# Optimization experiments

Hardware: AMD Instinct MI355X
Metric: run time of the kernel (lower is better)

The kernel has to match this reference:

```python
import jax, jax.numpy as jnp
import numpy as np
from jax import lax

B, Ht, Wt, C, NH, KV, FF = 32, 32, 32, 768, 12, 16, 4
HD = C // NH
EPS = 1e-5


def setup_inputs() -> dict:
    key = jax.random.key(0)
    ks = jax.random.split(key, 12)
    rn = lambda k, s, sc=0.02: jax.random.normal(k, s, jnp.float32) * sc
    inp = {"x": jax.random.normal(ks[0], (B, Ht * Wt, C), jnp.float32)}
    inp["ln1_g"] = jnp.ones((C,), jnp.float32)
    inp["ln1_b"] = jnp.zeros((C,), jnp.float32)
    for i, nm in enumerate(["q", "k", "v"]):
        inp[f"dw_w_{nm}"] = rn(ks[1 + i], (C, 1, 3, 3), 0.1)
        inp[f"dw_b_{nm}"] = jnp.zeros((C,), jnp.float32)
        inp[f"bn_g_{nm}"] = jnp.ones((C,), jnp.float32)
        inp[f"bn_b_{nm}"] = jnp.zeros((C,), jnp.float32)
        inp[f"bn_m_{nm}"] = jnp.zeros((C,), jnp.float32)
        inp[f"bn_v_{nm}"] = jnp.ones((C,), jnp.float32)
        inp[f"W_{nm}"] = rn(ks[4 + i], (C, C))
        inp[f"b_{nm}"] = jnp.zeros((C,), jnp.float32)
    inp["ln2_g"] = jnp.ones((C,), jnp.float32)
    inp["ln2_b"] = jnp.zeros((C,), jnp.float32)
    inp["W1"] = rn(ks[7], (FF * C, C))
    inp["b1"] = jnp.zeros((FF * C,), jnp.float32)
    inp["W2"] = rn(ks[8], (C, FF * C))
    inp["b2"] = jnp.zeros((C,), jnp.float32)
    return inp


def _ln(x, g, b):
    m = jnp.mean(x, -1, keepdims=True)
    v = jnp.var(x, -1, keepdims=True)
    return (x - m) * lax.rsqrt(v + EPS) * g + b


def _dw_branch(x4, w, bias, g, bb, m, v, stride):
    # depthwise conv (groups=C) -> ELU -> BatchNorm (eval) -> b (h w) c
    y = lax.conv_general_dilated(
        x4, w, (stride, stride), [(1, 1), (1, 1)],
        feature_group_count=C,
        dimension_numbers=("NCHW", "OIHW", "NCHW"),
    ) + bias[None, :, None, None]
    y = jax.nn.elu(y)
    y = (y - m[None, :, None, None]) * lax.rsqrt(v + EPS)[None, :, None, None] \
        * g[None, :, None, None] + bb[None, :, None, None]
    return y.reshape(B, C, -1).transpose(0, 2, 1)  # (B, n, C)


def _heads(t, Wm, bm):
    t = t @ Wm.T + bm                         # (B, n, C)
    n = t.shape[1]
    return t.reshape(B, n, NH, HD).transpose(0, 2, 1, 3)  # (B, H, n, d)


def reference(x, ln1_g, ln1_b,
              dw_w_q, dw_b_q, bn_g_q, bn_b_q, bn_m_q, bn_v_q, W_q, b_q,
              dw_w_k, dw_b_k, bn_g_k, bn_b_k, bn_m_k, bn_v_k, W_k, b_k,
              dw_w_v, dw_b_v, bn_g_v, bn_b_v, bn_m_v, bn_v_v, W_v, b_v,
              ln2_g, ln2_b, W1, b1, W2, b2):
    xn = _ln(x, ln1_g, ln1_b)
    x4 = xn.transpose(0, 2, 1).reshape(B, C, Ht, Wt)
    q = _heads(_dw_branch(x4, dw_w_q, dw_b_q, bn_g_q, bn_b_q, bn_m_q, bn_v_q, 1), W_q, b_q)
    k = _heads(_dw_branch(x4, dw_w_k, dw_b_k, bn_g_k, bn_b_k, bn_m_k, bn_v_k, 2), W_k, b_k)
    v = _heads(_dw_branch(x4, dw_w_v, dw_b_v, bn_g_v, bn_b_v, bn_m_v, bn_v_v, 2), W_v, b_v)
    scale = 1.0 / (HD ** 0.5)
    attn = jnp.einsum("bhnd,bhmd->bhnm", q, k) * scale
    attn = jax.nn.softmax(attn, axis=-1)
    o = jnp.einsum("bhnm,bhmd->bhnd", attn, v)
    o = o.transpose(0, 2, 1, 3).reshape(B, Ht * Wt, C)
    x = x + o  # DropPath is identity at inference
    h = _ln(x, ln2_g, ln2_b)
    h = jax.nn.gelu(h @ W1.T + b1, approximate=False) @ W2.T + b2
    return x + h
```

## Files before the change

### kernel.cpp

```cpp
#include <hip/hip_runtime.h>
#include <math.h>

#define NB   32
#define C_   768
#define NQ   1024
#define NKV  256
#define NH_  12
#define HD_  64
#define FFC  3072
#define EPS_ 1e-5f

typedef __attribute__((ext_vector_type(8))) _Float16 f16x8;
typedef __attribute__((ext_vector_type(4))) _Float16 f16x4;
typedef __attribute__((ext_vector_type(2))) _Float16 f16x2;
typedef __attribute__((ext_vector_type(4))) float    f32x4;

__device__ __forceinline__ void gload_lds16(const void* g, void* l) {
  __builtin_amdgcn_global_load_lds((const __attribute__((address_space(1))) void*)g,
                                   (__attribute__((address_space(3))) void*)l, 16, 0, 0);
}

__device__ __forceinline__ float gelu_f(float x) {
  return x / (1.f + __expf(-1.5957691216f * (x + 0.044715f * x * x * x)));
}

__global__ __launch_bounds__(256)
void ln_fwd_kernel(const float* __restrict__ x, const float* __restrict__ g,
                   const float* __restrict__ b, _Float16* __restrict__ out) {
  const int row = blockIdx.x;
  const float* xr = x + (size_t)row * C_;
  const int t = threadIdx.x;
  float v0 = xr[t], v1 = xr[t + 256], v2 = xr[t + 512];
  float s = v0 + v1 + v2;
  float q = v0 * v0 + v1 * v1 + v2 * v2;
#pragma unroll
  for (int m = 1; m < 64; m <<= 1) { s += __shfl_xor(s, m); q += __shfl_xor(q, m); }
  __shared__ float ls[4], lq[4];
  const int w = t >> 6, lane = t & 63;
  if (lane == 0) { ls[w] = s; lq[w] = q; }
  __syncthreads();
  s = ls[0] + ls[1] + ls[2] + ls[3];
  q = lq[0] + lq[1] + lq[2] + lq[3];
  const float mean = s * (1.f / C_);
  const float rstd = rsqrtf(q * (1.f / C_) - mean * mean + EPS_);
  _Float16* orow = out + (size_t)row * C_;
  orow[t]       = (_Float16)((v0 - mean) * rstd * g[t]       + b[t]);
  orow[t + 256] = (_Float16)((v1 - mean) * rstd * g[t + 256] + b[t + 256]);
  orow[t + 512] = (_Float16)((v2 - mean) * rstd * g[t + 512] + b[t + 512]);
}

__global__ __launch_bounds__(256)
void resln2_kernel(const float* __restrict__ x, const _Float16* __restrict__ o,
                   const float* __restrict__ g, const float* __restrict__ bb,
                   float* __restrict__ xr_out, _Float16* __restrict__ h) {
  const int row = blockIdx.x;
  const float* xp = x + (size_t)row * C_;
  const _Float16* op = o + (size_t)row * C_;
  const int t = threadIdx.x;
  float v[3]; float s = 0.f, q = 0.f;
#pragma unroll
  for (int i = 0; i < 3; i++) {
    int c = t + i * 256;
    v[i] = xp[c] + (float)op[c];
    s += v[i]; q += v[i] * v[i];
  }
#pragma unroll
  for (int m = 1; m < 64; m <<= 1) { s += __shfl_xor(s, m); q += __shfl_xor(q, m); }
  __shared__ float ls[4], lq[4];
  const int w = t >> 6, lane = t & 63;
  if (lane == 0) { ls[w] = s; lq[w] = q; }
  __syncthreads();
  s = ls[0] + ls[1] + ls[2] + ls[3];
  q = lq[0] + lq[1] + lq[2] + lq[3];
  const float mean = s * (1.f / C_);
  const float rstd = rsqrtf(q * (1.f / C_) - mean * mean + EPS_);
#pragma unroll
  for (int i = 0; i < 3; i++) {
    int c = t + i * 256;
    xr_out[(size_t)row * C_ + c] = v[i];
    h[(size_t)row * C_ + c] = (_Float16)((v[i] - mean) * rstd * g[c] + bb[c]);
  }
}

#define SZ_CC (C_ * C_)
#define SZ_CF (FFC * C_)
__global__ void cast_all_kernel(const float* __restrict__ Wq, const float* __restrict__ Wk,
                                const float* __restrict__ Wv, const float* __restrict__ W1,
                                const float* __restrict__ W2,
                                _Float16* __restrict__ oq, _Float16* __restrict__ ok,
                                _Float16* __restrict__ ov, _Float16* __restrict__ o1,
                                _Float16* __restrict__ o2) {
  const int total = 3 * SZ_CC + 2 * SZ_CF;
  int i = blockIdx.x * 256 + threadIdx.x;
  int stride = gridDim.x * 256;
  for (; i < total; i += stride) {
    if (i < SZ_CC)                     oq[i] = (_Float16)Wq[i];
    else if (i < 2 * SZ_CC)            ok[i - SZ_CC] = (_Float16)Wk[i - SZ_CC];
    else if (i < 3 * SZ_CC)            ov[i - 2 * SZ_CC] = (_Float16)Wv[i - 2 * SZ_CC];
    else if (i < 3 * SZ_CC + SZ_CF)    o1[i - 3 * SZ_CC] = (_Float16)W1[i - 3 * SZ_CC];
    else                               o2[i - 3 * SZ_CC - SZ_CF] = (_Float16)W2[i - 3 * SZ_CC - SZ_CF];
  }
}

__global__ __launch_bounds__(256)
void vtrans_kernel(const _Float16* __restrict__ vbuf, _Float16* __restrict__ vT) {
  const int b = blockIdx.z;
  const int c = blockIdx.y * 256 + threadIdx.x;
  const int kvb = blockIdx.x * 64;
#pragma unroll
  for (int kk = 0; kk < 8; kk++) {
    int kv0 = kvb + kk * 8;
    f16x8 v;
#pragma unroll
    for (int j = 0; j < 8; j++)
      v[j] = vbuf[(size_t)((b << 8) + kv0 + j) * C_ + c];
    *(f16x8*)(vT + ((size_t)(b * C_ + c) << 8) + kv0) = v;
  }
}

struct DwP { const float *w, *bias, *g, *b, *m, *v; };

__device__ __forceinline__ float elu_f(float x) {
  return x > 0.f ? x : __expf(x) - 1.f;
}

__global__ __launch_bounds__(384)
void dw_fused_kernel(const _Float16* __restrict__ xn, DwP pq, DwP pk, DwP pv,
                     _Float16* __restrict__ oq, _Float16* __restrict__ ok,
                     _Float16* __restrict__ ov) {
  const int i = blockIdx.x;
  const int b = blockIdx.z;
  const int c0 = 2 * threadIdx.x;
  const _Float16* xb = xn + (size_t)b * NQ * C_ + c0;

  float wqx[9], wqy[9], wkx[9], wky[9], wvx[9], wvy[9];
#pragma unroll
  for (int u = 0; u < 9; u++) {
    wqx[u] = pq.w[c0 * 9 + u]; wqy[u] = pq.w[(c0 + 1) * 9 + u];
    wkx[u] = pk.w[c0 * 9 + u]; wky[u] = pk.w[(c0 + 1) * 9 + u];
    wvx[u] = pv.w[c0 * 9 + u]; wvy[u] = pv.w[(c0 + 1) * 9 + u];
  }
  const float skqx = rsqrtf(pq.v[c0] + EPS_) * pq.g[c0], bnqx = pq.b[c0] - pq.m[c0] * skqx;
  const float skqy = rsqrtf(pq.v[c0+1] + EPS_) * pq.g[c0+1], bnqy = pq.b[c0+1] - pq.m[c0+1] * skqy;
  const float skkx = rsqrtf(pk.v[c0] + EPS_) * pk.g[c0], bnkx = pk.b[c0] - pk.m[c0] * skkx;
  const float skky = rsqrtf(pk.v[c0+1] + EPS_) * pk.g[c0+1], bnky = pk.b[c0+1] - pk.m[c0+1] * skky;
  const float skvx = rsqrtf(pv.v[c0] + EPS_) * pv.g[c0], bnvx = pv.b[c0] - pv.m[c0] * skvx;
  const float skvy = rsqrtf(pv.v[c0+1] + EPS_) * pv.g[c0+1], bnvy = pv.b[c0+1] - pv.m[c0+1] * skvy;
  const float cbqx = pq.bias[c0], cbqy = pq.bias[c0+1];
  const float cbkx = pk.bias[c0], cbky = pk.bias[c0+1];
  const float cbvx = pv.bias[c0], cbvy = pv.bias[c0+1];

  float tx[5][5], ty[5][5];
  auto ldc = [&](int s, int iw) {
    const bool cv = (iw >= 0 && iw < 32);
#pragma unroll
    for (int u = 0; u < 5; u++) {
      int ih = 2 * i - 1 + u;
      if (cv && ih >= 0 && ih < 32) {
        f16x2 p = *(const f16x2*)&xb[(size_t)(ih * 32 + iw) * C_];
        tx[u][s] = (float)p[0]; ty[u][s] = (float)p[1];
      } else { tx[u][s] = 0.f; ty[u][s] = 0.f; }
    }
  };

#pragma unroll
  for (int j = 0; j < 16; j++) {
    if (j == 0) {
      ldc(0, -1); ldc(1, 0); ldc(2, 1); ldc(3, 2); ldc(4, 3);
    } else {
#pragma unroll
      for (int u = 0; u < 5; u++) {
        tx[u][0] = tx[u][2]; tx[u][1] = tx[u][3]; tx[u][2] = tx[u][4];
        ty[u][0] = ty[u][2]; ty[u][1] = ty[u][3]; ty[u][2] = ty[u][4];
      }
      ldc(3, 2 * j + 2); ldc(4, 2 * j + 3);
    }
    float akx = cbkx, aky = cbky, avx = cbvx, avy = cbvy;
#pragma unroll
    for (int u = 0; u < 3; u++)
#pragma unroll
      for (int vv = 0; vv < 3; vv++) {
        akx += tx[u][vv] * wkx[u * 3 + vv]; aky += ty[u][vv] * wky[u * 3 + vv];
        avx += tx[u][vv] * wvx[u * 3 + vv]; avy += ty[u][vv] * wvy[u * 3 + vv];
      }
    f16x2 kv2, vv2;
    kv2[0] = (_Float16)(elu_f(akx) * skkx + bnkx);
    kv2[1] = (_Float16)(elu_f(aky) * skky + bnky);
    vv2[0] = (_Float16)(elu_f(avx) * skvx + bnvx);
    vv2[1] = (_Float16)(elu_f(avy) * skvy + bnvy);
    *(f16x2*)&ok[((size_t)b * NKV + i * 16 + j) * C_ + c0] = kv2;
    *(f16x2*)&ov[((size_t)b * NKV + i * 16 + j) * C_ + c0] = vv2;
#pragma unroll
    for (int a = 0; a < 2; a++)
#pragma unroll
      for (int b2 = 0; b2 < 2; b2++) {
        float aqx = cbqx, aqy = cbqy;
#pragma unroll
        for (int u = 0; u < 3; u++)
#pragma unroll
          for (int vv = 0; vv < 3; vv++) {
            aqx += tx[a + u][b2 + vv] * wqx[u * 3 + vv];
            aqy += ty[a + u][b2 + vv] * wqy[u * 3 + vv];
          }
        f16x2 q2;
        q2[0] = (_Float16)(elu_f(aqx) * skqx + bnqx);
        q2[1] = (_Float16)(elu_f(aqy) * skqy + bnqy);
        *(f16x2*)&oq[((size_t)b * NQ + (2 * i + a) * 32 + (2 * j + b2)) * C_ + c0] = q2;
      }
  }
}

__device__ __forceinline__ void stage_tile(const _Float16* __restrict__ src, int ldk,
                                           int row0, int kt, _Float16* lds, int w, int lane) {
#pragma unroll
  for (int it = 0; it < 4; it++) {
    int cid = (it * 4 + w) * 64 + lane;
    int row = cid >> 3, kg = cid & 7;
    int kgs = kg ^ (row & 7);
    const _Float16* g = src + (size_t)(row0 + row) * ldk + kt * 64 + kgs * 8;
    gload_lds16((const void*)g, (void*)((char*)lds + (it * 4 + w) * 1024));
  }
}

template <int EPI>
__device__ __forceinline__
void gemm_core(const _Float16* __restrict__ A, const _Float16* __restrict__ Bw,
               const float* __restrict__ bias,
               _Float16* __restrict__ outh, float* __restrict__ outf,
               int N, int K, int m0, int n0) {
  __shared__ __align__(16) _Float16 As[128 * 64];
  __shared__ __align__(16) _Float16 Bs[128 * 64];
  const int tid = threadIdx.x, w = tid >> 6, lane = tid & 63;
  const int wm = w >> 1, wn = w & 1;

  f32x4 acc[4][4];
#pragma unroll
  for (int i = 0; i < 4; i++)
#pragma unroll
    for (int j = 0; j < 4; j++)
#pragma unroll
      for (int r = 0; r < 4; r++) acc[i][j][r] = 0.f;

  const int NKT = K >> 6;
  for (int kt = 0; kt < NKT; kt++) {
    stage_tile(A, K, m0, kt, As, w, lane);
    stage_tile(Bw, K, n0, kt, Bs, w, lane);
    __syncthreads();
    f16x8 af[4][2], bfr[4][2];
#pragma unroll
    for (int mi = 0; mi < 4; mi++)
#pragma unroll
      for (int kh = 0; kh < 2; kh++) {
        int row = wm * 64 + mi * 16 + (lane & 15);
        int kg = kh * 4 + (lane >> 4);
        af[mi][kh] = *(const f16x8*)&As[row * 64 + ((kg ^ (row & 7)) << 3)];
      }
#pragma unroll
    for (int ni = 0; ni < 4; ni++)
#pragma unroll
      for (int kh = 0; kh < 2; kh++) {
        int row = wn * 64 + ni * 16 + (lane & 15);
        int kg = kh * 4 + (lane >> 4);
        bfr[ni][kh] = *(const f16x8*)&Bs[row * 64 + ((kg ^ (row & 7)) << 3)];
      }
    __builtin_amdgcn_s_setprio(1);
#pragma unroll
    for (int mi = 0; mi < 4; mi++)
#pragma unroll
      for (int ni = 0; ni < 4; ni++)
#pragma unroll
        for (int kh = 0; kh < 2; kh++)
          acc[mi][ni] = __builtin_amdgcn_mfma_f32_16x16x32_f16(af[mi][kh], bfr[ni][kh],
                                                               acc[mi][ni], 0, 0, 0);
    __builtin_amdgcn_s_setprio(0);
    __syncthreads();
  }
#pragma unroll
  for (int mi = 0; mi < 4; mi++)
#pragma unroll
    for (int ni = 0; ni < 4; ni++) {
      int col = n0 + wn * 64 + ni * 16 + (lane & 15);
      float bv = bias[col];
#pragma unroll
      for (int r = 0; r < 4; r++) {
        int rowg = m0 + wm * 64 + mi * 16 + (lane >> 4) * 4 + r;
        float val = acc[mi][ni][r] + bv;
        size_t idx = (size_t)rowg * N + col;
        if (EPI == 0)      outh[idx] = (_Float16)val;
        else if (EPI == 1) outh[idx] = (_Float16)gelu_f(val);
        else               outf[idx] += val;
      }
    }
}

template <int EPI>
__global__ __launch_bounds__(256, 3)
void gemm_f16(const _Float16* __restrict__ A, const _Float16* __restrict__ Bw,
              const float* __restrict__ bias,
              _Float16* __restrict__ outh, float* __restrict__ outf,
              int M, int N, int K, int NT) {
  const int nwg = gridDim.x, d = blockIdx.x;
  const int o = (d & 7) * (nwg >> 3) + (d >> 3);
  gemm_core<EPI>(A, Bw, bias, outh, outf, N, K, (o / NT) * 128, (o % NT) * 128);
}

__global__ __launch_bounds__(256, 3)
void gemm_kv(const _Float16* __restrict__ Ak, const _Float16* __restrict__ Wk,
             const float* __restrict__ bk, _Float16* __restrict__ outk,
             const _Float16* __restrict__ Av, const _Float16* __restrict__ Wv,
             const float* __restrict__ bv, _Float16* __restrict__ outv) {
  const int nwg = gridDim.x, d = blockIdx.x;
  int o = (d & 7) * (nwg >> 3) + (d >> 3);
  const bool isv = o >= 384;
  if (isv) o -= 384;
  const int m0 = (o / 6) * 128, n0 = (o % 6) * 128;
  if (isv) gemm_core<0>(Av, Wv, bv, outv, nullptr, C_, C_, m0, n0);
  else     gemm_core<0>(Ak, Wk, bk, outk, nullptr, C_, C_, m0, n0);
}

__global__ __launch_bounds__(512, 2)
void attn_kernel(const _Float16* __restrict__ Q, const _Float16* __restrict__ Kb,
                 const _Float16* __restrict__ vT, _Float16* __restrict__ O) {
  __shared__ __align__(16) _Float16 Klds[256 * 64];
  __shared__ __align__(16) _Float16 Vt[64 * 256];
  const int tid = threadIdx.x, w = tid >> 6, lane = tid & 63;
  const int hi = lane >> 4, lo = lane & 15;
  const int half = blockIdx.x & 1;
  const int h = (blockIdx.x >> 1) % NH_;
  const int b = blockIdx.x / (2 * NH_);

  const _Float16* qp = Q + (size_t)b * NQ * C_ + h * HD_;
  const _Float16* kp = Kb + (size_t)b * NKV * C_ + h * HD_;
  const _Float16* vp = vT + ((size_t)(b * C_ + h * HD_) << 8);

#pragma unroll
  for (int i = 0; i < 4; i++) {
    int cid = i * 512 + w * 64 + lane;
    int row = cid >> 3, kg = cid & 7;
    const _Float16* g = kp + (size_t)row * C_ + ((kg ^ (row & 7)) << 3);
    gload_lds16((const void*)g, (void*)((char*)Klds + (i * 512 + w * 64) * 16));
  }
#pragma unroll
  for (int i = 0; i < 4; i++) {
    int cid = i * 512 + w * 64 + lane;
    int row = cid >> 5, kg = cid & 31;
    const _Float16* g = vp + ((size_t)row << 8) + ((kg ^ (row & 7)) << 3);
    gload_lds16((const void*)g, (void*)((char*)Vt + (i * 512 + w * 64) * 16));
  }
  __syncthreads();

#pragma unroll
  for (int ti = 0; ti < 4; ti++) {
    const int q0 = half * 512 + w * 64 + ti * 16;
    f16x8 qf[2];
#pragma unroll
    for (int kh = 0; kh < 2; kh++)
      qf[kh] = *(const f16x8*)(qp + (size_t)(q0 + lo) * C_ + kh * 32 + hi * 8);
    f32x4 S[16];
#pragma unroll
    for (int nt = 0; nt < 16; nt++) {
      f32x4 s; s[0] = 0.f; s[1] = 0.f; s[2] = 0.f; s[3] = 0.f;
      const _Float16* krow = &Klds[(nt * 16 + lo) * 64];
#pragma unroll
      for (int kh = 0; kh < 2; kh++) {
        f16x8 kf = *(const f16x8*)&krow[((kh * 4 + hi) ^ (lo & 7)) << 3];
        s = __builtin_amdgcn_mfma_f32_16x16x32_f16(kf, qf[kh], s, 0, 0, 0);
      }
      S[nt] = s;
    }
    float mx = -1e30f;
#pragma unroll
    for (int nt = 0; nt < 16; nt++)
#pragma unroll
      for (int r = 0; r < 4; r++) { S[nt][r] *= 0.125f; mx = fmaxf(mx, S[nt][r]); }
    mx = fmaxf(mx, __shfl_xor(mx, 16));
    mx = fmaxf(mx, __shfl_xor(mx, 32));
    float sum = 0.f;
#pragma unroll
    for (int nt = 0; nt < 16; nt++)
#pragma unroll
      for (int r = 0; r < 4; r++) { float e = __expf(S[nt][r] - mx); S[nt][r] = e; sum += e; }
    sum += __shfl_xor(sum, 16);
    sum += __shfl_xor(sum, 32);
    const float inv = 1.f / sum;
    f16x8 pa8[8];
#pragma unroll
    for (int ntp = 0; ntp < 8; ntp++)
#pragma unroll
      for (int r = 0; r < 4; r++) {
        pa8[ntp][r]     = (_Float16)(S[2 * ntp][r] * inv);
        pa8[ntp][4 + r] = (_Float16)(S[2 * ntp + 1][r] * inv);
      }
    f32x4 acc[4];
#pragma unroll
    for (int dt = 0; dt < 4; dt++) { acc[dt][0] = 0.f; acc[dt][1] = 0.f; acc[dt][2] = 0.f; acc[dt][3] = 0.f; }
#pragma unroll
    for (int dt = 0; dt < 4; dt++) {
      const int d = dt * 16 + lo, sw = d & 7;
      const _Float16* vrow = &Vt[d * 256 + 4 * (hi & 1)];
#pragma unroll
      for (int ntp = 0; ntp < 8; ntp++) {
        f16x4 v0 = *(const f16x4*)&vrow[((4 * ntp + (hi >> 1)) ^ sw) << 3];
        f16x4 v1 = *(const f16x4*)&vrow[((4 * ntp + 2 + (hi >> 1)) ^ sw) << 3];
        f16x8 vt8;
#pragma unroll
        for (int r = 0; r < 4; r++) { vt8[r] = v0[r]; vt8[4 + r] = v1[r]; }
        acc[dt] = __builtin_amdgcn_mfma_f32_16x16x32_f16(pa8[ntp], vt8, acc[dt], 0, 0, 0);
      }
    }
#pragma unroll
    for (int dt = 0; dt < 4; dt++)
#pragma unroll
      for (int r = 0; r < 4; r++)
        O[(size_t)(b * NQ + q0 + 4 * hi + r) * C_ + h * HD_ + dt * 16 + lo] = (_Float16)acc[dt][r];
  }
}

extern "C" void kernel_launch(void* const* d_in, const int* in_sizes, int n_in,
                              void* d_out, int out_size, void* d_ws, size_t ws_size,
                              hipStream_t stream) {
  (void)in_sizes; (void)n_in; (void)out_size; (void)ws_size;
  const float* x    = (const float*)d_in[0];
  const float* ln1g = (const float*)d_in[1];
  const float* ln1b = (const float*)d_in[2];
  DwP pq { (const float*)d_in[3], (const float*)d_in[4], (const float*)d_in[5],
           (const float*)d_in[6], (const float*)d_in[7], (const float*)d_in[8] };
  const float* Wq = (const float*)d_in[9];  const float* bq = (const float*)d_in[10];
  DwP pk { (const float*)d_in[11], (const float*)d_in[12], (const float*)d_in[13],
           (const float*)d_in[14], (const float*)d_in[15], (const float*)d_in[16] };
  const float* Wk = (const float*)d_in[17]; const float* bk = (const float*)d_in[18];
  DwP pv { (const float*)d_in[19], (const float*)d_in[20], (const float*)d_in[21],
           (const float*)d_in[22], (const float*)d_in[23], (const float*)d_in[24] };
  const float* Wv = (const float*)d_in[25]; const float* bv = (const float*)d_in[26];
  const float* ln2g = (const float*)d_in[27];
  const float* ln2b = (const float*)d_in[28];
  const float* W1 = (const float*)d_in[29]; const float* b1 = (const float*)d_in[30];
  const float* W2 = (const float*)d_in[31]; const float* b2 = (const float*)d_in[32];

  char* ws = (char*)d_ws;
  _Float16* gbuf = (_Float16*)(ws + 0);
  _Float16* xn   = (_Float16*)(ws + 0);
  _Float16* qb   = (_Float16*)(ws + 50331648);
  _Float16* tk   = (_Float16*)(ws + 100663296);
  _Float16* tv   = (_Float16*)(ws + 113246208);
  _Float16* vTb  = tv;
  _Float16* kb   = (_Float16*)(ws + 125829120);
  _Float16* vbuf = (_Float16*)(ws + 138412032);
  _Float16* o    = (_Float16*)(ws + 150994944);
  _Float16* tq   = (_Float16*)(ws + 201326592);
  _Float16* hb   = tq;
  _Float16* wqh  = (_Float16*)(ws + 251658240);
  _Float16* wkh  = (_Float16*)(ws + 252837888);
  _Float16* wvh  = (_Float16*)(ws + 254017536);
  _Float16* w1h  = (_Float16*)(ws + 255197184);
  _Float16* w2h  = (_Float16*)(ws + 259915776);
  float* out = (float*)d_out;

  ln_fwd_kernel<<<NB * NQ, 256, 0, stream>>>(x, ln1g, ln1b, xn);
  cast_all_kernel<<<2048, 256, 0, stream>>>(Wq, Wk, Wv, W1, W2, wqh, wkh, wvh, w1h, w2h);
  dw_fused_kernel<<<dim3(16, 1, NB), 384, 0, stream>>>(xn, pq, pk, pv, tq, tk, tv);
  gemm_f16<0><<<1536, 256, 0, stream>>>(tq, wqh, bq, qb, nullptr, NB * NQ, C_, C_, 6);
  gemm_kv<<<768, 256, 0, stream>>>(tk, wkh, bk, kb, tv, wvh, bv, vbuf);
  vtrans_kernel<<<dim3(4, 3, NB), 256, 0, stream>>>(vbuf, vTb);
  attn_kernel<<<NB * NH_ * 2, 512, 0, stream>>>(qb, kb, vTb, o);
  resln2_kernel<<<NB * NQ, 256, 0, stream>>>(x, o, ln2g, ln2b, out, hb);
  gemm_f16<1><<<6144, 256, 0, stream>>>(hb, w1h, b1, gbuf, nullptr, NB * NQ, FFC, C_, 24);
  gemm_f16<2><<<1536, 256, 0, stream>>>(gbuf, w2h, b2, nullptr, out, NB * NQ, C_, FFC, 6);
}
```

Baseline: 786.6 us.

## Double-buffer GEMM LDS tiles and split depthwise conv across column halves

The GEMM core now keeps two LDS buffers per operand and prefetches the next K tile with global_load_lds while MFMAs run on the current one, replacing the load-then-sync-then-compute sequence with one wait and barrier per iteration. Occupancy hint drops from 3 to 2 blocks per CU to fit the doubled LDS. The depthwise conv kernel is split across two column halves via blockIdx.y, doubling its grid for more parallelism at the cost of reloading a few halo columns.

```diff
diff --git a/kernel.cpp b/kernel.cpp
--- a/kernel.cpp
+++ b/kernel.cpp
@@ -129,6 +129,7 @@
                      _Float16* __restrict__ oq, _Float16* __restrict__ ok,
                      _Float16* __restrict__ ov) {
   const int i = blockIdx.x;
+  const int jh = blockIdx.y;
   const int b = blockIdx.z;
   const int c0 = 2 * threadIdx.x;
   const _Float16* xb = xn + (size_t)b * NQ * C_ + c0;
@@ -163,10 +164,13 @@
     }
   };
 
-#pragma unroll
-  for (int j = 0; j < 16; j++) {
-    if (j == 0) {
-      ldc(0, -1); ldc(1, 0); ldc(2, 1); ldc(3, 2); ldc(4, 3);
+  const int j0 = jh * 8;
+#pragma unroll
+  for (int jj = 0; jj < 8; jj++) {
+    const int j = j0 + jj;
+    if (jj == 0) {
+      ldc(0, 2 * j0 - 1); ldc(1, 2 * j0); ldc(2, 2 * j0 + 1);
+      ldc(3, 2 * j0 + 2); ldc(4, 2 * j0 + 3);
     } else {
 #pragma unroll
       for (int u = 0; u < 5; u++) {
@@ -228,8 +232,8 @@
                const float* __restrict__ bias,
                _Float16* __restrict__ outh, float* __restrict__ outf,
                int N, int K, int m0, int n0) {
-  __shared__ __align__(16) _Float16 As[128 * 64];
-  __shared__ __align__(16) _Float16 Bs[128 * 64];
+  __shared__ __align__(16) _Float16 As[2][128 * 64];
+  __shared__ __align__(16) _Float16 Bs[2][128 * 64];
   const int tid = threadIdx.x, w = tid >> 6, lane = tid & 63;
   const int wm = w >> 1, wn = w & 1;
 
@@ -241,11 +245,18 @@
 #pragma unroll
       for (int r = 0; r < 4; r++) acc[i][j][r] = 0.f;
 
+  stage_tile(A, K, m0, 0, As[0], w, lane);
+  stage_tile(Bw, K, n0, 0, Bs[0], w, lane);
+  asm volatile("s_waitcnt vmcnt(0)" ::: "memory");
+  __builtin_amdgcn_s_barrier();
+
   const int NKT = K >> 6;
+  int cur = 0;
   for (int kt = 0; kt < NKT; kt++) {
-    stage_tile(A, K, m0, kt, As, w, lane);
-    stage_tile(Bw, K, n0, kt, Bs, w, lane);
-    __syncthreads();
+    if (kt + 1 < NKT) {
+      stage_tile(A, K, m0, kt + 1, As[cur ^ 1], w, lane);
+      stage_tile(Bw, K, n0, kt + 1, Bs[cur ^ 1], w, lane);
+    }
     f16x8 af[4][2], bfr[4][2];
 #pragma unroll
     for (int mi = 0; mi < 4; mi++)
@@ -253,7 +264,7 @@
       for (int kh = 0; kh < 2; kh++) {
         int row = wm * 64 + mi * 16 + (lane & 15);
         int kg = kh * 4 + (lane >> 4);
-        af[mi][kh] = *(const f16x8*)&As[row * 64 + ((kg ^ (row & 7)) << 3)];
+        af[mi][kh] = *(const f16x8*)&As[cur][row * 64 + ((kg ^ (row & 7)) << 3)];
       }
 #pragma unroll
     for (int ni = 0; ni < 4; ni++)
@@ -261,7 +272,7 @@
       for (int kh = 0; kh < 2; kh++) {
         int row = wn * 64 + ni * 16 + (lane & 15);
         int kg = kh * 4 + (lane >> 4);
-        bfr[ni][kh] = *(const f16x8*)&Bs[row * 64 + ((kg ^ (row & 7)) << 3)];
+        bfr[ni][kh] = *(const f16x8*)&Bs[cur][row * 64 + ((kg ^ (row & 7)) << 3)];
       }
     __builtin_amdgcn_s_setprio(1);
 #pragma unroll
@@ -273,7 +284,9 @@
           acc[mi][ni] = __builtin_amdgcn_mfma_f32_16x16x32_f16(af[mi][kh], bfr[ni][kh],
                                                                acc[mi][ni], 0, 0, 0);
     __builtin_amdgcn_s_setprio(0);
-    __syncthreads();
+    asm volatile("s_waitcnt vmcnt(0)" ::: "memory");
+    __builtin_amdgcn_s_barrier();
+    cur ^= 1;
   }
 #pragma unroll
   for (int mi = 0; mi < 4; mi++)
@@ -294,7 +307,7 @@
 }
 
 template <int EPI>
-__global__ __launch_bounds__(256, 3)
+__global__ __launch_bounds__(256, 2)
 void gemm_f16(const _Float16* __restrict__ A, const _Float16* __restrict__ Bw,
               const float* __restrict__ bias,
               _Float16* __restrict__ outh, float* __restrict__ outf,
@@ -304,7 +317,7 @@
   gemm_core<EPI>(A, Bw, bias, outh, outf, N, K, (o / NT) * 128, (o % NT) * 128);
 }
 
-__global__ __launch_bounds__(256, 3)
+__global__ __launch_bounds__(256, 2)
 void gemm_kv(const _Float16* __restrict__ Ak, const _Float16* __restrict__ Wk,
              const float* __restrict__ bk, _Float16* __restrict__ outk,
              const _Float16* __restrict__ Av, const _Float16* __restrict__ Wv,
@@ -458,7 +471,7 @@
 
   ln_fwd_kernel<<<NB * NQ, 256, 0, stream>>>(x, ln1g, ln1b, xn);
   cast_all_kernel<<<2048, 256, 0, stream>>>(Wq, Wk, Wv, W1, W2, wqh, wkh, wvh, w1h, w2h);
-  dw_fused_kernel<<<dim3(16, 1, NB), 384, 0, stream>>>(xn, pq, pk, pv, tq, tk, tv);
+  dw_fused_kernel<<<dim3(16, 2, NB), 384, 0, stream>>>(xn, pq, pk, pv, tq, tk, tv);
   gemm_f16<0><<<1536, 256, 0, stream>>>(tq, wqh, bq, qb, nullptr, NB * NQ, C_, C_, 6);
   gemm_kv<<<768, 256, 0, stream>>>(tk, wkh, bk, kb, tv, wvh, bv, vbuf);
   vtrans_kernel<<<dim3(4, 3, NB), 256, 0, stream>>>(vbuf, vTb);
```

Result: slower. 885.2 us (+12.5%).

## Use 256x256 double-buffered GEMM tiles for MLP and split depthwise conv over columns

Applied to the files above, without the earlier changes.

Adds a 512-thread GEMM kernel with 256x256 output tiles and double-buffered LDS staging through async global-to-LDS loads, and uses it for the two MLP GEMMs (FC1 with GELU, FC2 with residual accumulate). Larger tiles raise arithmetic intensity and cut redundant global reads, and prefetching two k-steps ahead overlaps loads with MFMA work. The depthwise conv kernel is also split into two column halves to double its grid and parallelism. The cost is higher register and LDS use (128KB LDS per block), which lowers occupancy, and FC2 launches only 384 blocks, which may leave some CUs idle.

```diff
diff --git a/kernel.cpp b/kernel.cpp
--- a/kernel.cpp
+++ b/kernel.cpp
@@ -129,6 +129,7 @@
                      _Float16* __restrict__ oq, _Float16* __restrict__ ok,
                      _Float16* __restrict__ ov) {
   const int i = blockIdx.x;
+  const int jh = blockIdx.y;
   const int b = blockIdx.z;
   const int c0 = 2 * threadIdx.x;
   const _Float16* xb = xn + (size_t)b * NQ * C_ + c0;
@@ -163,10 +164,13 @@
     }
   };
 
-#pragma unroll
-  for (int j = 0; j < 16; j++) {
-    if (j == 0) {
-      ldc(0, -1); ldc(1, 0); ldc(2, 1); ldc(3, 2); ldc(4, 3);
+  const int j0 = jh * 8;
+#pragma unroll
+  for (int jj = 0; jj < 8; jj++) {
+    const int j = j0 + jj;
+    if (jj == 0) {
+      ldc(0, 2 * j0 - 1); ldc(1, 2 * j0); ldc(2, 2 * j0 + 1);
+      ldc(3, 2 * j0 + 2); ldc(4, 2 * j0 + 3);
     } else {
 #pragma unroll
       for (int u = 0; u < 5; u++) {
@@ -222,12 +226,10 @@
   }
 }
 
-template <int EPI>
 __device__ __forceinline__
-void gemm_core(const _Float16* __restrict__ A, const _Float16* __restrict__ Bw,
-               const float* __restrict__ bias,
-               _Float16* __restrict__ outh, float* __restrict__ outf,
-               int N, int K, int m0, int n0) {
+void gemm_core128(const _Float16* __restrict__ A, const _Float16* __restrict__ Bw,
+                  const float* __restrict__ bias, _Float16* __restrict__ outh,
+                  int N, int K, int m0, int n0) {
   __shared__ __align__(16) _Float16 As[128 * 64];
   __shared__ __align__(16) _Float16 Bs[128 * 64];
   const int tid = threadIdx.x, w = tid >> 6, lane = tid & 63;
@@ -284,24 +286,18 @@
 #pragma unroll
       for (int r = 0; r < 4; r++) {
         int rowg = m0 + wm * 64 + mi * 16 + (lane >> 4) * 4 + r;
-        float val = acc[mi][ni][r] + bv;
-        size_t idx = (size_t)rowg * N + col;
-        if (EPI == 0)      outh[idx] = (_Float16)val;
-        else if (EPI == 1) outh[idx] = (_Float16)gelu_f(val);
-        else               outf[idx] += val;
+        outh[(size_t)rowg * N + col] = (_Float16)(acc[mi][ni][r] + bv);
       }
     }
 }
 
-template <int EPI>
 __global__ __launch_bounds__(256, 3)
-void gemm_f16(const _Float16* __restrict__ A, const _Float16* __restrict__ Bw,
-              const float* __restrict__ bias,
-              _Float16* __restrict__ outh, float* __restrict__ outf,
-              int M, int N, int K, int NT) {
+void gemm_q(const _Float16* __restrict__ A, const _Float16* __restrict__ Bw,
+            const float* __restrict__ bias, _Float16* __restrict__ outh,
+            int N, int K, int NT) {
   const int nwg = gridDim.x, d = blockIdx.x;
   const int o = (d & 7) * (nwg >> 3) + (d >> 3);
-  gemm_core<EPI>(A, Bw, bias, outh, outf, N, K, (o / NT) * 128, (o % NT) * 128);
+  gemm_core128(A, Bw, bias, outh, N, K, (o / NT) * 128, (o % NT) * 128);
 }
 
 __global__ __launch_bounds__(256, 3)
@@ -314,8 +310,120 @@
   const bool isv = o >= 384;
   if (isv) o -= 384;
   const int m0 = (o / 6) * 128, n0 = (o % 6) * 128;
-  if (isv) gemm_core<0>(Av, Wv, bv, outv, nullptr, C_, C_, m0, n0);
-  else     gemm_core<0>(Ak, Wk, bk, outk, nullptr, C_, C_, m0, n0);
+  if (isv) gemm_core128(Av, Wv, bv, outv, C_, C_, m0, n0);
+  else     gemm_core128(Ak, Wk, bk, outk, C_, C_, m0, n0);
+}
+
+__device__ __forceinline__ void stage256(const _Float16* __restrict__ src, int ldk,
+                                         int row0, int kt, _Float16* lds, int w, int lane) {
+#pragma unroll
+  for (int it = 0; it < 4; it++) {
+    int cid = it * 512 + w * 64 + lane;
+    int row = cid >> 3, kg = cid & 7;
+    const _Float16* g = src + (size_t)(row0 + row) * ldk + kt * 64 + ((kg ^ (row & 7)) << 3);
+    gload_lds16((const void*)g, (void*)((char*)lds + (it * 512 + w * 64) * 16));
+  }
+}
+
+template <int EPI>
+__global__ __launch_bounds__(512, 2)
+void gemm256(const _Float16* __restrict__ A, const _Float16* __restrict__ Bw,
+             const float* __restrict__ bias,
+             _Float16* __restrict__ outh, float* __restrict__ outf,
+             int N, int K, int NT) {
+  __shared__ __align__(16) _Float16 As[2][256 * 64];
+  __shared__ __align__(16) _Float16 Bs[2][256 * 64];
+  const int tid = threadIdx.x, w = tid >> 6, lane = tid & 63;
+  const int wm = w >> 2, wn = w & 3;
+  const int hi = lane >> 4, lo = lane & 15;
+  const int nwg = gridDim.x, d = blockIdx.x;
+  const int o = (d & 7) * (nwg >> 3) + (d >> 3);
+  const int m0 = (o / NT) * 256, n0 = (o % NT) * 256;
+
+  f32x4 acc[8][4];
+#pragma unroll
+  for (int i = 0; i < 8; i++)
+#pragma unroll
+    for (int j = 0; j < 4; j++)
+#pragma unroll
+      for (int r = 0; r < 4; r++) acc[i][j][r] = 0.f;
+
+  stage256(A, K, m0, 0, As[0], w, lane);
+  stage256(Bw, K, n0, 0, Bs[0], w, lane);
+  stage256(A, K, m0, 1, As[1], w, lane);
+  stage256(Bw, K, n0, 1, Bs[1], w, lane);
+  asm volatile("s_waitcnt vmcnt(8)" ::: "memory");
+  __builtin_amdgcn_s_barrier();
+
+  const int NKT = K >> 6;
+  int cur = 0;
+  for (int kt = 0; kt < NKT; kt++) {
+    const _Float16* as = As[cur];
+    const _Float16* bs = Bs[cur];
+#pragma unroll
+    for (int mh = 0; mh < 2; mh++)
+#pragma unroll
+      for (int nh = 0; nh < 2; nh++) {
+        f16x8 af[4][2], bf[2][2];
+#pragma unroll
+        for (int mi = 0; mi < 4; mi++)
+#pragma unroll
+          for (int kh = 0; kh < 2; kh++) {
+            int row = wm * 128 + mh * 64 + mi * 16 + lo;
+            int kg = kh * 4 + hi;
+            af[mi][kh] = *(const f16x8*)&as[row * 64 + ((kg ^ (row & 7)) << 3)];
+          }
+#pragma unroll
+        for (int ni = 0; ni < 2; ni++)
+#pragma unroll
+          for (int kh = 0; kh < 2; kh++) {
+            int row = wn * 64 + nh * 32 + ni * 16 + lo;
+            int kg = kh * 4 + hi;
+            bf[ni][kh] = *(const f16x8*)&bs[row * 64 + ((kg ^ (row & 7)) << 3)];
+          }
+        __builtin_amdgcn_s_setprio(1);
+#pragma unroll
+        for (int mi = 0; mi < 4; mi++)
+#pragma unroll
+          for (int ni = 0; ni < 2; ni++)
+#pragma unroll
+            for (int kh = 0; kh < 2; kh++)
+              acc[mh * 4 + mi][nh * 2 + ni] =
+                  __builtin_amdgcn_mfma_f32_16x16x32_f16(af[mi][kh], bf[ni][kh],
+                                                         acc[mh * 4 + mi][nh * 2 + ni], 0, 0, 0);
+        __builtin_amdgcn_s_setprio(0);
+        __builtin_amdgcn_sched_barrier(0);
+      }
+    __builtin_amdgcn_s_barrier();
+    if (kt + 2 < NKT) {
+      stage256(A, K, m0, kt + 2, As[cur], w, lane);
+      stage256(Bw, K, n0, kt + 2, Bs[cur], w, lane);
+      asm volatile("s_waitcnt vmcnt(8)" ::: "memory");
+    } else {
+      asm volatile("s_waitcnt vmcnt(0)" ::: "memory");
+    }
+    __builtin_amdgcn_s_barrier();
+    cur ^= 1;
+  }
+#pragma unroll
+  for (int mh = 0; mh < 2; mh++)
+#pragma unroll
+    for (int mi = 0; mi < 4; mi++)
+#pragma unroll
+      for (int nh = 0; nh < 2; nh++)
+#pragma unroll
+        for (int ni = 0; ni < 2; ni++) {
+          int col = n0 + wn * 64 + nh * 32 + ni * 16 + lo;
+          float bv = bias[col];
+#pragma unroll
+          for (int r = 0; r < 4; r++) {
+            int rowg = m0 + wm * 128 + mh * 64 + mi * 16 + hi * 4 + r;
+            float val = acc[mh * 4 + mi][nh * 2 + ni][r] + bv;
+            size_t idx = (size_t)rowg * N + col;
+            if (EPI == 1) outh[idx] = (_Float16)gelu_f(val);
+            else          outf[idx] += val;
+          }
+        }
 }
 
 __global__ __launch_bounds__(512, 2)
@@ -458,12 +566,12 @@
 
   ln_fwd_kernel<<<NB * NQ, 256, 0, stream>>>(x, ln1g, ln1b, xn);
   cast_all_kernel<<<2048, 256, 0, stream>>>(Wq, Wk, Wv, W1, W2, wqh, wkh, wvh, w1h, w2h);
-  dw_fused_kernel<<<dim3(16, 1, NB), 384, 0, stream>>>(xn, pq, pk, pv, tq, tk, tv);
-  gemm_f16<0><<<1536, 256, 0, stream>>>(tq, wqh, bq, qb, nullptr, NB * NQ, C_, C_, 6);
+  dw_fused_kernel<<<dim3(16, 2, NB), 384, 0, stream>>>(xn, pq, pk, pv, tq, tk, tv);
+  gemm_q<<<1536, 256, 0, stream>>>(tq, wqh, bq, qb, C_, C_, 6);
   gemm_kv<<<768, 256, 0, stream>>>(tk, wkh, bk, kb, tv, wvh, bv, vbuf);
   vtrans_kernel<<<dim3(4, 3, NB), 256, 0, stream>>>(vbuf, vTb);
   attn_kernel<<<NB * NH_ * 2, 512, 0, stream>>>(qb, kb, vTb, o);
   resln2_kernel<<<NB * NQ, 256, 0, stream>>>(x, o, ln2g, ln2b, out, hb);
-  gemm_f16<1><<<6144, 256, 0, stream>>>(hb, w1h, b1, gbuf, nullptr, NB * NQ, FFC, C_, 24);
-  gemm_f16<2><<<1536, 256, 0, stream>>>(gbuf, w2h, b2, nullptr, out, NB * NQ, C_, FFC, 6);
-}
+  gemm256<1><<<1536, 512, 0, stream>>>(hb, w1h, b1, gbuf, nullptr, FFC, C_, 12);
+  gemm256<2><<<384, 512, 0, stream>>>(gbuf, w2h, b2, nullptr, out, C_, FFC, 3);
+}
```

New measurement: 967.1 us. +22.9%, slower.
